# Performance work log

Hardware: AMD Instinct MI355X
Metric: run time of the kernel (lower is better)

Reference implementation:

```python
import jax, jax.numpy as jnp
import numpy as np

N, E = 50000, 800000
INF, ONF, HNF = 64, 64, 128
EPS = 1e-8


def qmul(p, q):
    # roma XYZW Hamilton product
    px, py, pz, pw = p[:, 0], p[:, 1], p[:, 2], p[:, 3]
    qx, qy, qz, qw = q[:, 0], q[:, 1], q[:, 2], q[:, 3]
    return jnp.stack([
        pw * qx + px * qw + py * qz - pz * qy,
        pw * qy - px * qz + py * qw + pz * qx,
        pw * qz + px * qy - py * qx + pz * qw,
        pw * qw - px * qx - py * qy - pz * qz,
    ], axis=1)


def qinv(q):
    conj = jnp.concatenate([-q[:, :3], q[:, 3:]], axis=1)
    return conj / jnp.sum(q * q, axis=1, keepdims=True)


def rot_apply(q, v):
    # rotate v by unit quaternion q (XYZW)
    qv, w = q[:, :3], q[:, 3:4]
    t = 2.0 * jnp.cross(qv, v)
    return v + w * t + jnp.cross(qv, t)


def quat_exponential(im):
    r = jnp.linalg.norm(im, axis=1, keepdims=True)
    u = im / r
    return jnp.concatenate([u * jnp.sin(r), jnp.cos(r)], axis=1)


def seg_sum(data, ids, n):
    return jax.ops.segment_sum(data, ids, num_segments=n)


def seg_mean(data, ids, n):
    s = seg_sum(data, ids, n)
    c = seg_sum(jnp.ones_like(data), ids, n)
    return s / jnp.maximum(c, 1.0)


def setup_inputs() -> dict:
    key = jax.random.key(0)
    ks = jax.random.split(key, 24)
    h = jax.random.normal(ks[0], (N, INF), jnp.float32)
    coord = jax.random.normal(ks[1], (N, 3), jnp.float32)
    q = jax.random.normal(ks[2], (N, 4), jnp.float32)
    quat = q / jnp.linalg.norm(q, axis=1, keepdims=True)
    edge_index = jax.random.randint(ks[3], (2, E), 0, N)

    def lin(k, fi, fo, scale=None):
        s = (1.0 / np.sqrt(fi)) if scale is None else scale
        return jax.random.uniform(k, (fi, fo), jnp.float32, -s, s)

    ein = 2 * INF + 8  # source, target, radial(1), quat_prod(4), unit_vecs(3)
    params = dict(
        We1=lin(ks[4], ein, HNF), be1=jnp.zeros((HNF,), jnp.float32),
        We2=lin(ks[5], HNF, HNF), be2=jnp.zeros((HNF,), jnp.float32),
        Wn1=lin(ks[6], HNF + INF, HNF), bn1=jnp.zeros((HNF,), jnp.float32),
        Wn2=lin(ks[7], HNF, ONF), bn2=jnp.zeros((ONF,), jnp.float32),
        Wc1=lin(ks[8], HNF, HNF), bc1=jnp.zeros((HNF,), jnp.float32),
        wc2=lin(ks[9], HNF, 1, scale=0.001),  # xavier gain 0.001, no bias
        Wq1=lin(ks[10], HNF, HNF), bq1=jnp.zeros((HNF,), jnp.float32),
        Wq2=lin(ks[11], HNF, 3), bq2=jnp.zeros((3,), jnp.float32),
    )
    return dict(h=h, edge_index=edge_index, coord=coord, quat=quat, **params)


def reference(h, edge_index, coord, quat,
              We1, be1, We2, be2, Wn1, bn1, Wn2, bn2,
              Wc1, bc1, wc2, Wq1, bq1, Wq2, bq2):
    silu = jax.nn.silu
    row, col = edge_index[0], edge_index[1]

    # invariants
    coord_diff = coord[row] - coord[col]                       # [E,3]
    qi = qinv(quat)
    quat_prod = qmul(qi[row], quat[col])                       # [E,4]
    radial = jnp.sum(coord_diff ** 2, axis=1, keepdims=True)   # [E,1]
    norm = jnp.sqrt(radial) + EPS
    unit_vecs = -rot_apply(qi[row], coord_diff / norm)         # [E,3]

    # edge model
    ein = jnp.concatenate([h[row], h[col], radial, quat_prod, unit_vecs], axis=1)
    edge_feat = silu(silu(ein @ We1 + be1) @ We2 + be2)        # [E,HNF]

    # coord model (mean agg)
    trans = coord_diff * (silu(edge_feat @ Wc1 + bc1) @ wc2)   # [E,3]
    coord = coord + seg_mean(trans, row, N)

    # quat model (mean agg)
    tan_vecs = silu(edge_feat @ Wq1 + bq1) @ Wq2 + bq2         # [E,3]
    rots = quat_exponential(seg_mean(tan_vecs, row, N))
    quat = qmul(quat, rots)

    # node model (sum agg), residual
    agg = seg_sum(edge_feat, row, N)
    nin = jnp.concatenate([h, agg], axis=1)
    h = h + (silu(nin @ Wn1 + bn1) @ Wn2 + bn2)
    return (h, coord, quat)
```

## Files before the change

### kernel.cpp

```cpp
#include <hip/hip_runtime.h>
#include <hip/hip_bf16.h>
#include <math.h>


#define N_NODES 50000
#define N_EDGES 800000
#define ASTR 172
#define NSTR 204

typedef __attribute__((ext_vector_type(4))) float f32x4;
typedef __attribute__((ext_vector_type(8))) short bf16x8;
typedef __attribute__((ext_vector_type(4))) unsigned short u16x4;
typedef __attribute__((ext_vector_type(8))) unsigned short u16x8;

static __device__ __forceinline__ unsigned short f2bf(float f) {
  return __builtin_bit_cast(unsigned short, __float2bfloat16(f));
}
static __device__ __forceinline__ float bf2f(unsigned short s) {
  unsigned int u = ((unsigned int)s) << 16;
  return __builtin_bit_cast(float, u);
}
static __device__ __forceinline__ float silu_f(float x) {
  return x * __builtin_amdgcn_rcpf(1.0f + __expf(-x));
}
static __device__ __forceinline__ void atomic_pk_add_bf16(unsigned int* addr,
                                                          float lo, float hi) {
  const unsigned int pk = ((unsigned int)f2bf(hi) << 16) | (unsigned int)f2bf(lo);
  asm volatile("global_atomic_pk_add_bf16 %0, %1, off"
               :: "v"((unsigned long long)(uintptr_t)addr), "v"(pk)
               : "memory");
}

__global__ void hist_kernel(const int* __restrict__ ei, int* __restrict__ cursor) {
  int e = blockIdx.x * blockDim.x + threadIdx.x;
  if (e < N_EDGES) atomicAdd(&cursor[ei[e]], 1);
}

__global__ void scan_kernel(int* __restrict__ cursor, int* __restrict__ offsets) {
  __shared__ int s[1024];
  const int t = threadIdx.x;
  const int C = 49;
  const int base = t * C;
  int sum = 0;
  for (int i = 0; i < C; ++i) {
    int n = base + i;
    if (n < N_NODES) sum += cursor[n];
  }
  s[t] = sum;
  __syncthreads();
  for (int d = 1; d < 1024; d <<= 1) {
    int v = (t >= d) ? s[t - d] : 0;
    __syncthreads();
    s[t] += v;
    __syncthreads();
  }
  int run = s[t] - sum;
  for (int i = 0; i < C; ++i) {
    int n = base + i;
    if (n < N_NODES) {
      int d = cursor[n];
      offsets[n] = run;
      cursor[n] = run;
      run += d;
    }
  }
  if (t == 1023) offsets[N_NODES] = run;
}

__global__ void scatter_kernel(const int* __restrict__ ei, int* __restrict__ cursor,
                               int2* __restrict__ rc2) {
  int e = blockIdx.x * blockDim.x + threadIdx.x;
  if (e < N_EDGES) {
    int r = ei[e];
    int pos = atomicAdd(&cursor[r], 1);
    int2 v; v.x = r; v.y = ei[N_EDGES + e];
    rc2[pos] = v;
  }
}

__global__ void swz_kernel(const float* __restrict__ src, unsigned short* __restrict__ dst,
                           int K, int NOUT, int KT, int NCT) {
  int idx = blockIdx.x * blockDim.x + threadIdx.x;
  if (idx >= KT * NCT * 64) return;
  int lane = idx & 63, blk = idx >> 6;
  int ct = blk % NCT, kt = blk / NCT;
  int col = ct * 16 + (lane & 15);
  int kb = kt * 32 + (lane >> 4) * 8;
  u16x8 o;
  #pragma unroll
  for (int j = 0; j < 8; ++j) {
    int k = kb + j;
    o[j] = (k < K) ? f2bf(src[(size_t)k * NOUT + col]) : (unsigned short)0;
  }
  *(u16x8*)(dst + (size_t)idx * 8) = o;
}

template <int KT, int NCT>
static __device__ __forceinline__ void mmW2(const unsigned short* __restrict__ a0,
                                            const unsigned short* __restrict__ a1,
                                            int lk,
                                            const unsigned short* __restrict__ Wb,
                                            int lane, f32x4* acc0, f32x4* acc1) {
  const f32x4 zero = {0.f, 0.f, 0.f, 0.f};
  #pragma unroll
  for (int ct = 0; ct < NCT; ++ct) { acc0[ct] = zero; acc1[ct] = zero; }
  __builtin_amdgcn_s_setprio(1);
  #pragma unroll
  for (int kt = 0; kt < KT; ++kt) {
    bf16x8 x0 = *(const bf16x8*)(a0 + kt*32 + lk*8);
    bf16x8 x1 = *(const bf16x8*)(a1 + kt*32 + lk*8);
    const u16x8* bb = (const u16x8*)Wb + (size_t)(kt*NCT)*64 + lane;
    #pragma unroll
    for (int ct = 0; ct < NCT; ++ct) {
      bf16x8 w = *(const bf16x8*)(bb + (size_t)ct*64);
      acc0[ct] = __builtin_amdgcn_mfma_f32_16x16x32_bf16(w, x0, acc0[ct], 0, 0, 0);
      acc1[ct] = __builtin_amdgcn_mfma_f32_16x16x32_bf16(w, x1, acc1[ct], 0, 0, 0);
    }
  }
  __builtin_amdgcn_s_setprio(0);
}

__global__ __launch_bounds__(256, 3) void edge_kernel(
    const float* __restrict__ h,
    const float* __restrict__ coord, const float* __restrict__ quat,
    const int2* __restrict__ rc2,
    const unsigned short* __restrict__ We1b, const unsigned short* __restrict__ We2b,
    const unsigned short* __restrict__ Wc1b, const unsigned short* __restrict__ Wq1b,
    const float* __restrict__ be1, const float* __restrict__ be2,
    const float* __restrict__ bc1, const float* __restrict__ wc2,
    const float* __restrict__ bq1, const float* __restrict__ Wq2,
    const float* __restrict__ bq2,
    unsigned int* __restrict__ agg32, float* __restrict__ transS,
    float* __restrict__ tanS, float* __restrict__ cnt)
{
  __shared__ __align__(16) unsigned short AF[128 * ASTR];

  const int tid = threadIdx.x;
  const int wv = tid >> 6, lane = tid & 63;
  const int lr = lane & 15, lk = lane >> 4;
  const int row0 = wv*32 + lr, row1 = row0 + 16;

  const int xcd = blockIdx.x & 7, idx = blockIdx.x >> 3;
  const int q = 781, rem = 2;
  const int bid = (xcd < rem ? xcd*(q+1) : rem*(q+1) + (xcd-rem)*q) + idx;
  const int e0 = bid * 128;

  const int2 p0v = rc2[e0 + row0];
  const int2 p1v = rc2[e0 + row1];
  const int r0 = p0v.x, c0 = p0v.y, r1 = p1v.x, c1 = p1v.y;

  {
    const float* hs0 = h + (size_t)(lk < 2 ? r0 : c0) * 64 + (lk & 1) * 32;
    const float* hs1 = h + (size_t)(lk < 2 ? r1 : c1) * 64 + (lk & 1) * 32;
    const int cb = lk * 32;
    #pragma unroll
    for (int j = 0; j < 32; j += 4) {
      f32x4 v0 = *(const f32x4*)(hs0 + j);
      f32x4 v1 = *(const f32x4*)(hs1 + j);
      u16x4 q0, q1;
      #pragma unroll
      for (int i = 0; i < 4; ++i) { q0[i] = f2bf(v0[i]); q1[i] = f2bf(v1[i]); }
      *(u16x4*)&AF[row0*ASTR + cb + j] = q0;
      *(u16x4*)&AF[row1*ASTR + cb + j] = q1;
    }
  }
  const float cdx0 = coord[r0*3+0] - coord[c0*3+0];
  const float cdy0 = coord[r0*3+1] - coord[c0*3+1];
  const float cdz0 = coord[r0*3+2] - coord[c0*3+2];
  const float cdx1 = coord[r1*3+0] - coord[c1*3+0];
  const float cdy1 = coord[r1*3+1] - coord[c1*3+1];
  const float cdz1 = coord[r1*3+2] - coord[c1*3+2];
  if (lk < 2) {
    const int gr = lk ? r1 : r0, gc = lk ? c1 : c0, grow = lk ? row1 : row0;
    const float gx = lk ? cdx1 : cdx0, gy = lk ? cdy1 : cdy0, gz = lk ? cdz1 : cdz0;
    const float radial = gx*gx + gy*gy + gz*gz;
    const float nrm = sqrtf(radial) + 1e-8f;
    const f32x4 qr4 = *(const f32x4*)&quat[gr*4];
    const f32x4 qc4 = *(const f32x4*)&quat[gc*4];
    const float qix = -qr4[0], qiy = -qr4[1], qiz = -qr4[2], qiw = qr4[3];
    const float qcx = qc4[0], qcy = qc4[1], qcz = qc4[2], qcw = qc4[3];
    const float qpx = qiw*qcx + qix*qcw + qiy*qcz - qiz*qcy;
    const float qpy = qiw*qcy - qix*qcz + qiy*qcw + qiz*qcx;
    const float qpz = qiw*qcz + qix*qcy - qiy*qcx + qiz*qcw;
    const float qpw = qiw*qcw - qix*qcx - qiy*qcy - qiz*qcz;
    const float rinv = __builtin_amdgcn_rcpf(nrm);
    const float vx = gx*rinv, vy = gy*rinv, vz = gz*rinv;
    const float tx = 2.f*(qiy*vz - qiz*vy);
    const float ty = 2.f*(qiz*vx - qix*vz);
    const float tz = 2.f*(qix*vy - qiy*vx);
    const float ux = -(vx + qiw*tx + (qiy*tz - qiz*ty));
    const float uy = -(vy + qiw*ty + (qiz*tx - qix*tz));
    const float uz = -(vz + qiw*tz + (qix*ty - qiy*tx));
    u16x4 f0, f1;
    f0[0] = f2bf(radial); f0[1] = f2bf(qpx); f0[2] = f2bf(qpy); f0[3] = f2bf(qpz);
    f1[0] = f2bf(qpw);    f1[1] = f2bf(ux);  f1[2] = f2bf(uy);  f1[3] = f2bf(uz);
    *(u16x4*)&AF[grow*ASTR + 128] = f0;
    *(u16x4*)&AF[grow*ASTR + 132] = f1;
    const u16x4 z4 = {0, 0, 0, 0};
    #pragma unroll
    for (int j = 136; j < 160; j += 4) *(u16x4*)&AF[grow*ASTR + j] = z4;
  }

  f32x4 acc0[8], acc1[8];

  mmW2<5,8>(AF + row0*ASTR, AF + row1*ASTR, lk, We1b, lane, acc0, acc1);
  #pragma unroll
  for (int ct = 0; ct < 8; ++ct) {
    const int ocb = ct*16 + lk*4;
    const f32x4 b4 = *(const f32x4*)&be1[ocb];
    u16x4 k0, k1;
    #pragma unroll
    for (int i = 0; i < 4; ++i) {
      k0[i] = f2bf(silu_f(acc0[ct][i] + b4[i]));
      k1[i] = f2bf(silu_f(acc1[ct][i] + b4[i]));
    }
    *(u16x4*)&AF[row0*ASTR + ocb] = k0;
    *(u16x4*)&AF[row1*ASTR + ocb] = k1;
  }

  mmW2<4,8>(AF + row0*ASTR, AF + row1*ASTR, lk, We2b, lane, acc0, acc1);
  #pragma unroll
  for (int ct = 0; ct < 8; ++ct) {
    const int ocb = ct*16 + lk*4;
    const f32x4 b4 = *(const f32x4*)&be2[ocb];
    u16x4 k0, k1;
    #pragma unroll
    for (int i = 0; i < 4; ++i) {
      k0[i] = f2bf(silu_f(acc0[ct][i] + b4[i]));
      k1[i] = f2bf(silu_f(acc1[ct][i] + b4[i]));
    }
    *(u16x4*)&AF[row0*ASTR + ocb] = k0;
    *(u16x4*)&AF[row1*ASTR + ocb] = k1;
  }

  float pcs0 = 0.f, pcs1 = 0.f;
  mmW2<4,8>(AF + row0*ASTR, AF + row1*ASTR, lk, Wc1b, lane, acc0, acc1);
  #pragma unroll
  for (int ct = 0; ct < 8; ++ct) {
    const int ocb = ct*16 + lk*4;
    const f32x4 b4 = *(const f32x4*)&bc1[ocb];
    const f32x4 w4 = *(const f32x4*)&wc2[ocb];
    #pragma unroll
    for (int i = 0; i < 4; ++i) {
      pcs0 += silu_f(acc0[ct][i] + b4[i]) * w4[i];
      pcs1 += silu_f(acc1[ct][i] + b4[i]) * w4[i];
    }
  }
  pcs0 += __shfl_xor(pcs0, 16);  pcs0 += __shfl_xor(pcs0, 32);
  pcs1 += __shfl_xor(pcs1, 16);  pcs1 += __shfl_xor(pcs1, 32);

  float p00 = 0.f, p10 = 0.f, p20 = 0.f;
  float p01 = 0.f, p11 = 0.f, p21 = 0.f;
  mmW2<4,8>(AF + row0*ASTR, AF + row1*ASTR, lk, Wq1b, lane, acc0, acc1);
  #pragma unroll
  for (int ct = 0; ct < 8; ++ct) {
    const int ocb = ct*16 + lk*4;
    const f32x4 b4 = *(const f32x4*)&bq1[ocb];
    const float* wq = &Wq2[ocb*3];
    const f32x4 qa = *(const f32x4*)(wq);
    const f32x4 qb = *(const f32x4*)(wq + 4);
    const f32x4 qc = *(const f32x4*)(wq + 8);
    {
      const float v0 = silu_f(acc0[ct][0] + b4[0]);
      const float v1 = silu_f(acc0[ct][1] + b4[1]);
      const float v2 = silu_f(acc0[ct][2] + b4[2]);
      const float v3 = silu_f(acc0[ct][3] + b4[3]);
      p00 += v0*qa[0] + v1*qa[3] + v2*qb[2] + v3*qc[1];
      p10 += v0*qa[1] + v1*qb[0] + v2*qb[3] + v3*qc[2];
      p20 += v0*qa[2] + v1*qb[1] + v2*qc[0] + v3*qc[3];
    }
    {
      const float v0 = silu_f(acc1[ct][0] + b4[0]);
      const float v1 = silu_f(acc1[ct][1] + b4[1]);
      const float v2 = silu_f(acc1[ct][2] + b4[2]);
      const float v3 = silu_f(acc1[ct][3] + b4[3]);
      p01 += v0*qa[0] + v1*qa[3] + v2*qb[2] + v3*qc[1];
      p11 += v0*qa[1] + v1*qb[0] + v2*qb[3] + v3*qc[2];
      p21 += v0*qa[2] + v1*qb[1] + v2*qc[0] + v3*qc[3];
    }
  }
  p00 += __shfl_xor(p00, 16);  p00 += __shfl_xor(p00, 32);
  p10 += __shfl_xor(p10, 16);  p10 += __shfl_xor(p10, 32);
  p20 += __shfl_xor(p20, 16);  p20 += __shfl_xor(p20, 32);
  p01 += __shfl_xor(p01, 16);  p01 += __shfl_xor(p01, 32);
  p11 += __shfl_xor(p11, 16);  p11 += __shfl_xor(p11, 32);
  p21 += __shfl_xor(p21, 16);  p21 += __shfl_xor(p21, 32);

  #pragma unroll
  for (int g = 0; g < 2; ++g) {
    const int rg = g ? r1 : r0;
    const int rUp = __shfl_up(rg, 1, 16);
    const int rDn = __shfl_down(rg, 1, 16);
    const bool head = (lr == 0) || (rUp != rg);
    const bool tail = (lr == 15) || (rDn != rg);
    float v1, v2;
    if (lk == 3) { v1 = 1.0f; v2 = 0.f; }
    else {
      const float cdj = (lk == 0) ? (g ? cdx1 : cdx0)
                      : (lk == 1) ? (g ? cdy1 : cdy0) : (g ? cdz1 : cdz0);
      const float pj  = (lk == 0) ? (g ? p01 : p00)
                      : (lk == 1) ? (g ? p11 : p10) : (g ? p21 : p20);
      v1 = cdj * (g ? pcs1 : pcs0);
      v2 = pj + bq2[lk];
    }
    int f = head ? 1 : 0;
    #pragma unroll
    for (int d = 1; d < 16; d <<= 1) {
      const float o1 = __shfl_up(v1, d, 16);
      const float o2 = __shfl_up(v2, d, 16);
      const int   of = __shfl_up(f,  d, 16);
      if (lr >= d) {
        if (!f) { v1 += o1; v2 += o2; }
        f |= of;
      }
    }
    if (tail) {
      if (lk == 3) {
        atomicAdd(&cnt[rg], v1);
      } else {
        atomicAdd(&transS[rg*3 + lk], v1);
        atomicAdd(&tanS[rg*3 + lk], v2);
      }
    }
  }

  {
    float rl_ = 0.f, rh_ = 0.f;
    int prev = __shfl(r0, 0, 16);
    #pragma unroll
    for (int k2 = 0; k2 < 32; ++k2) {
      const int rr = (k2 < 16) ? __shfl(r0, k2, 16) : __shfl(r1, k2 - 16, 16);
      if (rr != prev) {
        atomic_pk_add_bf16(&agg32[(size_t)prev*64 + lane], rl_, rh_);
        rl_ = 0.f; rh_ = 0.f; prev = rr;
      }
      const unsigned int u = *(const unsigned int*)&AF[(wv*32 + k2)*ASTR + 2*lane];
      rl_ += bf2f((unsigned short)(u & 0xffffu));
      rh_ += bf2f((unsigned short)(u >> 16));
    }
    atomic_pk_add_bf16(&agg32[(size_t)prev*64 + lane], rl_, rh_);
  }
}

__global__ __launch_bounds__(256, 4) void node_kernel(
    const float* __restrict__ h, const float* __restrict__ coord,
    const float* __restrict__ quat,
    const unsigned short* __restrict__ aggb, const float* __restrict__ transS,
    const float* __restrict__ tanS, const float* __restrict__ cnt,
    const unsigned short* __restrict__ Wn1b, const unsigned short* __restrict__ Wn2b,
    const float* __restrict__ bn1, const float* __restrict__ bn2,
    float* __restrict__ out_h, float* __restrict__ out_c, float* __restrict__ out_q)
{
  __shared__ unsigned short A_[64][NSTR];
  const int tid = threadIdx.x;
  const int n0 = blockIdx.x * 64;

  {
    const int row = tid >> 2, sub = tid & 3;
    const int n = n0 + row;
    if (n < N_NODES) {
      if (sub < 2) {
        const float* hp = h + (size_t)n*64 + sub*32;
        #pragma unroll
        for (int j = 0; j < 32; j += 4) {
          f32x4 v = *(const f32x4*)(hp + j);
          u16x4 p;
          p[0] = f2bf(v[0]); p[1] = f2bf(v[1]); p[2] = f2bf(v[2]); p[3] = f2bf(v[3]);
          *(u16x4*)&A_[row][sub*32 + j] = p;
        }
      } else {
        const unsigned short* ap = aggb + (size_t)n*128 + (sub - 2)*64;
        #pragma unroll
        for (int j = 0; j < 64; j += 8)
          *(u16x8*)&A_[row][64 + (sub - 2)*64 + j] = *(const u16x8*)(ap + j);
      }
    } else {
      const u16x4 z4 = {0, 0, 0, 0};
      if (sub < 2) {
        #pragma unroll
        for (int j = 0; j < 32; j += 4) *(u16x4*)&A_[row][sub*32 + j] = z4;
      } else {
        #pragma unroll
        for (int j = 0; j < 64; j += 4) *(u16x4*)&A_[row][64 + (sub - 2)*64 + j] = z4;
      }
    }
  }
  __syncthreads();

  const int wv = tid >> 6, lane = tid & 63;
  const int lr = lane & 15, lk = lane >> 4;
  const int nrow = wv*16 + lr;
  f32x4 acc[8];

  {
    const f32x4 zero = {0.f, 0.f, 0.f, 0.f};
    #pragma unroll
    for (int ct = 0; ct < 8; ++ct) acc[ct] = zero;
    #pragma unroll
    for (int kt = 0; kt < 6; ++kt) {
      bf16x8 act = *(const bf16x8*)&A_[nrow][kt*32 + lk*8];
      const u16x8* bb = (const u16x8*)Wn1b + (size_t)(kt*8)*64 + lane;
      #pragma unroll
      for (int ct = 0; ct < 8; ++ct) {
        bf16x8 w = *(const bf16x8*)(bb + (size_t)ct*64);
        acc[ct] = __builtin_amdgcn_mfma_f32_16x16x32_bf16(w, act, acc[ct], 0, 0, 0);
      }
    }
  }
  #pragma unroll
  for (int ct = 0; ct < 8; ++ct) {
    const int ocb = ct*16 + lk*4;
    const f32x4 b4 = *(const f32x4*)&bn1[ocb];
    u16x4 pk;
    #pragma unroll
    for (int i = 0; i < 4; ++i) pk[i] = f2bf(silu_f(acc[ct][i] + b4[i]));
    *(u16x4*)&A_[nrow][ocb] = pk;
  }

  f32x4 acc2[4];
  {
    const f32x4 zero = {0.f, 0.f, 0.f, 0.f};
    #pragma unroll
    for (int ct = 0; ct < 4; ++ct) acc2[ct] = zero;
    #pragma unroll
    for (int kt = 0; kt < 4; ++kt) {
      bf16x8 act = *(const bf16x8*)&A_[nrow][kt*32 + lk*8];
      const u16x8* bb = (const u16x8*)Wn2b + (size_t)(kt*4)*64 + lane;
      #pragma unroll
      for (int ct = 0; ct < 4; ++ct) {
        bf16x8 w = *(const bf16x8*)(bb + (size_t)ct*64);
        acc2[ct] = __builtin_amdgcn_mfma_f32_16x16x32_bf16(w, act, acc2[ct], 0, 0, 0);
      }
    }
  }
  const int n = n0 + nrow;
  if (n < N_NODES) {
    #pragma unroll
    for (int ct = 0; ct < 4; ++ct) {
      const int ocb = ct*16 + lk*4;
      const f32x4 b4 = *(const f32x4*)&bn2[ocb];
      const f32x4 h4 = *(const f32x4*)&h[(size_t)n*64 + ocb];
      f32x4 o;
      #pragma unroll
      for (int i = 0; i < 4; ++i) o[i] = h4[i] + acc2[ct][i] + b4[i];
      *(f32x4*)&out_h[(size_t)n*64 + ocb] = o;
    }
  }

  if (tid < 64) {
    const int nn = n0 + tid;
    if (nn < N_NODES) {
      const float cm = fmaxf(cnt[nn], 1.0f);
      const float inv = 1.0f / cm;
      out_c[nn*3+0] = coord[nn*3+0] + transS[nn*3+0]*inv;
      out_c[nn*3+1] = coord[nn*3+1] + transS[nn*3+1]*inv;
      out_c[nn*3+2] = coord[nn*3+2] + transS[nn*3+2]*inv;
      const float ix = tanS[nn*3+0]*inv, iy = tanS[nn*3+1]*inv, iz = tanS[nn*3+2]*inv;
      const float rr = sqrtf(ix*ix + iy*iy + iz*iz);
      const float s = sinf(rr) / rr;
      const float rx = ix*s, ry = iy*s, rz = iz*s, rw = cosf(rr);
      const float px = quat[nn*4+0], py = quat[nn*4+1], pz = quat[nn*4+2], pw = quat[nn*4+3];
      out_q[nn*4+0] = pw*rx + px*rw + py*rz - pz*ry;
      out_q[nn*4+1] = pw*ry - px*rz + py*rw + pz*rx;
      out_q[nn*4+2] = pw*rz + px*ry - py*rx + pz*rw;
      out_q[nn*4+3] = pw*rw - px*rx - py*ry - pz*rz;
    }
  }
}

extern "C" void kernel_launch(void* const* d_in, const int* in_sizes, int n_in,
                              void* d_out, int out_size, void* d_ws, size_t ws_size,
                              hipStream_t stream) {
  (void)in_sizes; (void)n_in; (void)out_size; (void)ws_size;
  const float* h     = (const float*)d_in[0];
  const int*   ei    = (const int*)d_in[1];
  const float* coord = (const float*)d_in[2];
  const float* quat  = (const float*)d_in[3];
  const float* We1 = (const float*)d_in[4];  const float* be1 = (const float*)d_in[5];
  const float* We2 = (const float*)d_in[6];  const float* be2 = (const float*)d_in[7];
  const float* Wn1 = (const float*)d_in[8];  const float* bn1 = (const float*)d_in[9];
  const float* Wn2 = (const float*)d_in[10]; const float* bn2 = (const float*)d_in[11];
  const float* Wc1 = (const float*)d_in[12]; const float* bc1 = (const float*)d_in[13];
  const float* wc2 = (const float*)d_in[14];
  const float* Wq1 = (const float*)d_in[15]; const float* bq1 = (const float*)d_in[16];
  const float* Wq2 = (const float*)d_in[17]; const float* bq2 = (const float*)d_in[18];

  char* ws = (char*)d_ws;
  unsigned int* agg32  = (unsigned int*)(ws);
  unsigned short* aggb = (unsigned short*)(ws);
  float* transS = (float*)(ws + 12800000);
  float* tanS   = (float*)(ws + 13400000);
  float* cnt    = (float*)(ws + 14000000);
  int*   cursor = (int*)  (ws + 14200000);
  int*   offs   = (int*)  (ws + 14400000);
  int2*  rc2    = (int2*) (ws + 14600064);
  unsigned short* We1b = (unsigned short*)(ws + 21000064);
  unsigned short* We2b = We1b + 5*8*64*8;
  unsigned short* Wc1b = We2b + 4*8*64*8;
  unsigned short* Wq1b = Wc1b + 4*8*64*8;
  unsigned short* Wn1b = Wq1b + 4*8*64*8;
  unsigned short* Wn2b = Wn1b + 6*8*64*8;

  hipMemsetAsync(ws, 0, 14400000, stream);
  swz_kernel<<<(5*8*64 + 255)/256, 256, 0, stream>>>(We1, We1b, 136, 128, 5, 8);
  swz_kernel<<<(4*8*64 + 255)/256, 256, 0, stream>>>(We2, We2b, 128, 128, 4, 8);
  swz_kernel<<<(4*8*64 + 255)/256, 256, 0, stream>>>(Wc1, Wc1b, 128, 128, 4, 8);
  swz_kernel<<<(4*8*64 + 255)/256, 256, 0, stream>>>(Wq1, Wq1b, 128, 128, 4, 8);
  swz_kernel<<<(6*8*64 + 255)/256, 256, 0, stream>>>(Wn1, Wn1b, 192, 128, 6, 8);
  swz_kernel<<<(4*4*64 + 255)/256, 256, 0, stream>>>(Wn2, Wn2b, 128, 64, 4, 4);
  hist_kernel<<<(N_EDGES + 255)/256, 256, 0, stream>>>(ei, cursor);
  scan_kernel<<<1, 1024, 0, stream>>>(cursor, offs);
  scatter_kernel<<<(N_EDGES + 255)/256, 256, 0, stream>>>(ei, cursor, rc2);

  edge_kernel<<<N_EDGES/128, 256, 0, stream>>>(
      h, coord, quat, rc2, We1b, We2b, Wc1b, Wq1b,
      be1, be2, bc1, wc2, bq1, Wq2, bq2, agg32, transS, tanS, cnt);

  float* out_h = (float*)d_out;
  float* out_c = out_h + (size_t)N_NODES*64;
  float* out_q = out_c + (size_t)N_NODES*3;
  node_kernel<<<(N_NODES + 63)/64, 256, 0, stream>>>(
      h, coord, quat, aggb, transS, tanS, cnt, Wn1b, Wn2b, bn1, bn2,
      out_h, out_c, out_q);
}
```

Before: 524.3 us.

## Fuse weight swizzle and histogram into one prep kernel; halve edge block size

Merges the six weight-swizzle launches and the degree-histogram launch into one prep kernel, and drops the unused offsets array, to cut launch count. The edge kernel now runs 64-edge blocks of 128 threads with half the shared memory, which gives twice as many blocks and finer XCD balancing. Row indices in the aggregation loop are now broadcast with readlane instead of shuffles. Smaller blocks raise occupancy but add per-block overhead and more boundary atomics.

```diff
diff --git a/kernel.cpp b/kernel.cpp
--- a/kernel.cpp
+++ b/kernel.cpp
@@ -31,12 +31,46 @@
                : "memory");
 }
 
-__global__ void hist_kernel(const int* __restrict__ ei, int* __restrict__ cursor) {
-  int e = blockIdx.x * blockDim.x + threadIdx.x;
-  if (e < N_EDGES) atomicAdd(&cursor[ei[e]], 1);
-}
-
-__global__ void scan_kernel(int* __restrict__ cursor, int* __restrict__ offsets) {
+static __device__ __forceinline__ void swz_do(const float* __restrict__ src,
+                                              unsigned short* __restrict__ dst,
+                                              int K, int NOUT, int NCT, int idx) {
+  int lane = idx & 63, blk = idx >> 6;
+  int ct = blk % NCT, kt = blk / NCT;
+  int col = ct * 16 + (lane & 15);
+  int kb = kt * 32 + (lane >> 4) * 8;
+  u16x8 o;
+  #pragma unroll
+  for (int j = 0; j < 8; ++j) {
+    int k = kb + j;
+    o[j] = (k < K) ? f2bf(src[(size_t)k * NOUT + col]) : (unsigned short)0;
+  }
+  *(u16x8*)(dst + (size_t)idx * 8) = o;
+}
+
+__global__ __launch_bounds__(256) void prep1_kernel(
+    const float* __restrict__ We1, const float* __restrict__ We2,
+    const float* __restrict__ Wc1, const float* __restrict__ Wq1,
+    const float* __restrict__ Wn1, const float* __restrict__ Wn2,
+    unsigned short* __restrict__ We1b, unsigned short* __restrict__ We2b,
+    unsigned short* __restrict__ Wc1b, unsigned short* __restrict__ Wq1b,
+    unsigned short* __restrict__ Wn1b, unsigned short* __restrict__ Wn2b,
+    const int* __restrict__ ei, int* __restrict__ cursor)
+{
+  const int b = blockIdx.x, t = threadIdx.x;
+  if (b >= 50) {
+    const int e = (b - 50) * 256 + t;
+    if (e < N_EDGES) atomicAdd(&cursor[ei[e]], 1);
+    return;
+  }
+  if (b < 10)       swz_do(We1, We1b, 136, 128, 8, b*256 + t);
+  else if (b < 18)  swz_do(We2, We2b, 128, 128, 8, (b-10)*256 + t);
+  else if (b < 26)  swz_do(Wc1, Wc1b, 128, 128, 8, (b-18)*256 + t);
+  else if (b < 34)  swz_do(Wq1, Wq1b, 128, 128, 8, (b-26)*256 + t);
+  else if (b < 46) { int i = (b-34)*256 + t; if (i < 3072) swz_do(Wn1, Wn1b, 192, 128, 8, i); }
+  else              swz_do(Wn2, Wn2b, 128, 64, 4, (b-46)*256 + t);
+}
+
+__global__ void scan_kernel(int* __restrict__ cursor) {
   __shared__ int s[1024];
   const int t = threadIdx.x;
   const int C = 49;
@@ -59,12 +93,10 @@
     int n = base + i;
     if (n < N_NODES) {
       int d = cursor[n];
-      offsets[n] = run;
       cursor[n] = run;
       run += d;
     }
   }
-  if (t == 1023) offsets[N_NODES] = run;
 }
 
 __global__ void scatter_kernel(const int* __restrict__ ei, int* __restrict__ cursor,
@@ -78,23 +110,6 @@
   }
 }
 
-__global__ void swz_kernel(const float* __restrict__ src, unsigned short* __restrict__ dst,
-                           int K, int NOUT, int KT, int NCT) {
-  int idx = blockIdx.x * blockDim.x + threadIdx.x;
-  if (idx >= KT * NCT * 64) return;
-  int lane = idx & 63, blk = idx >> 6;
-  int ct = blk % NCT, kt = blk / NCT;
-  int col = ct * 16 + (lane & 15);
-  int kb = kt * 32 + (lane >> 4) * 8;
-  u16x8 o;
-  #pragma unroll
-  for (int j = 0; j < 8; ++j) {
-    int k = kb + j;
-    o[j] = (k < K) ? f2bf(src[(size_t)k * NOUT + col]) : (unsigned short)0;
-  }
-  *(u16x8*)(dst + (size_t)idx * 8) = o;
-}
-
 template <int KT, int NCT>
 static __device__ __forceinline__ void mmW2(const unsigned short* __restrict__ a0,
                                             const unsigned short* __restrict__ a1,
@@ -120,7 +135,7 @@
   __builtin_amdgcn_s_setprio(0);
 }
 
-__global__ __launch_bounds__(256, 3) void edge_kernel(
+__global__ __launch_bounds__(128, 3) void edge_kernel(
     const float* __restrict__ h,
     const float* __restrict__ coord, const float* __restrict__ quat,
     const int2* __restrict__ rc2,
@@ -133,7 +148,7 @@
     unsigned int* __restrict__ agg32, float* __restrict__ transS,
     float* __restrict__ tanS, float* __restrict__ cnt)
 {
-  __shared__ __align__(16) unsigned short AF[128 * ASTR];
+  __shared__ __align__(16) unsigned short AF[64 * ASTR];
 
   const int tid = threadIdx.x;
   const int wv = tid >> 6, lane = tid & 63;
@@ -141,9 +156,9 @@
   const int row0 = wv*32 + lr, row1 = row0 + 16;
 
   const int xcd = blockIdx.x & 7, idx = blockIdx.x >> 3;
-  const int q = 781, rem = 2;
+  const int q = 1562, rem = 4;
   const int bid = (xcd < rem ? xcd*(q+1) : rem*(q+1) + (xcd-rem)*q) + idx;
-  const int e0 = bid * 128;
+  const int e0 = bid * 64;
 
   const int2 p0v = rc2[e0 + row0];
   const int2 p1v = rc2[e0 + row1];
@@ -326,10 +341,11 @@
 
   {
     float rl_ = 0.f, rh_ = 0.f;
-    int prev = __shfl(r0, 0, 16);
+    int prev = __builtin_amdgcn_readlane(r0, 0);
     #pragma unroll
     for (int k2 = 0; k2 < 32; ++k2) {
-      const int rr = (k2 < 16) ? __shfl(r0, k2, 16) : __shfl(r1, k2 - 16, 16);
+      const int rr = (k2 < 16) ? __builtin_amdgcn_readlane(r0, k2)
+                               : __builtin_amdgcn_readlane(r1, k2 - 16);
       if (rr != prev) {
         atomic_pk_add_bf16(&agg32[(size_t)prev*64 + lane], rl_, rh_);
         rl_ = 0.f; rh_ = 0.f; prev = rr;
@@ -492,7 +508,6 @@
   float* tanS   = (float*)(ws + 13400000);
   float* cnt    = (float*)(ws + 14000000);
   int*   cursor = (int*)  (ws + 14200000);
-  int*   offs   = (int*)  (ws + 14400000);
   int2*  rc2    = (int2*) (ws + 14600064);
   unsigned short* We1b = (unsigned short*)(ws + 21000064);
   unsigned short* We2b = We1b + 5*8*64*8;
@@ -502,17 +517,13 @@
   unsigned short* Wn2b = Wn1b + 6*8*64*8;
 
   hipMemsetAsync(ws, 0, 14400000, stream);
-  swz_kernel<<<(5*8*64 + 255)/256, 256, 0, stream>>>(We1, We1b, 136, 128, 5, 8);
-  swz_kernel<<<(4*8*64 + 255)/256, 256, 0, stream>>>(We2, We2b, 128, 128, 4, 8);
-  swz_kernel<<<(4*8*64 + 255)/256, 256, 0, stream>>>(Wc1, Wc1b, 128, 128, 4, 8);
-  swz_kernel<<<(4*8*64 + 255)/256, 256, 0, stream>>>(Wq1, Wq1b, 128, 128, 4, 8);
-  swz_kernel<<<(6*8*64 + 255)/256, 256, 0, stream>>>(Wn1, Wn1b, 192, 128, 6, 8);
-  swz_kernel<<<(4*4*64 + 255)/256, 256, 0, stream>>>(Wn2, Wn2b, 128, 64, 4, 4);
-  hist_kernel<<<(N_EDGES + 255)/256, 256, 0, stream>>>(ei, cursor);
-  scan_kernel<<<1, 1024, 0, stream>>>(cursor, offs);
+  prep1_kernel<<<50 + (N_EDGES + 255)/256, 256, 0, stream>>>(
+      We1, We2, Wc1, Wq1, Wn1, Wn2, We1b, We2b, Wc1b, Wq1b, Wn1b, Wn2b,
+      ei, cursor);
+  scan_kernel<<<1, 1024, 0, stream>>>(cursor);
   scatter_kernel<<<(N_EDGES + 255)/256, 256, 0, stream>>>(ei, cursor, rc2);
 
-  edge_kernel<<<N_EDGES/128, 256, 0, stream>>>(
+  edge_kernel<<<N_EDGES/64, 128, 0, stream>>>(
       h, coord, quat, rc2, We1b, We2b, Wc1b, Wq1b,
       be1, be2, bc1, wc2, bq1, Wq2, bq2, agg32, transS, tanS, cnt);
 
```

Measured after the change: 477.2 us. 9.0% less time.
